# Kernel optimization log

Measured on AMD Instinct MI355X. Metric: run time of the kernel, lower is better.

Reference implementation:

```python
import jax, jax.numpy as jnp
import numpy as np

B, L, D, C, NL = 32, 512, 768, 97, 2  # batch, seq_len, hidden, class_nums, gat_layers


def setup_inputs() -> dict:
    key = jax.random.key(0)
    ks = jax.random.split(key, 16)

    def n(k, shape, scale=0.02):
        return jax.random.normal(k, shape, dtype=jnp.float32) * scale

    return dict(
        x=n(ks[0], (B, L, D), 1.0),                 # encoder output
        pos1=jnp.ones((B, L), jnp.float32),          # entity-1 position mask
        pos2=jnp.ones((B, L), jnp.float32),          # entity-2 position mask
        mask=jnp.ones((B, L), jnp.int32),            # attention mask (1 = keep)
        emb=n(ks[1], (C, D), 1.0),                   # relation label embedding table
        rel_w=n(ks[2], (D, D)), rel_b=jnp.zeros((D,), jnp.float32),
        # per-layer, per-RA (axis1: 0=ra1, 1=ra2) parameters
        qw=n(ks[3], (NL, 2, D, D)), qb=jnp.zeros((NL, 2, D), jnp.float32),
        kw=n(ks[4], (NL, 2, D, D)), kb=jnp.zeros((NL, 2, D), jnp.float32),
        vw=n(ks[5], (NL, 2, D, D)), vb=jnp.zeros((NL, 2, D), jnp.float32),
        sw=n(ks[6], (NL, 2, 2 * D)), sb=jnp.zeros((NL, 2), jnp.float32),   # score: Linear(2d,1)
        gw=n(ks[7], (NL, 2, 2 * D)), gb=jnp.zeros((NL, 2), jnp.float32),   # gate:  Linear(2d,1)
        fc1_w=n(ks[8], (3 * D, D)), fc1_b=jnp.zeros((D,), jnp.float32),
        fc2_w=n(ks[9], (D,)), fc2_b=jnp.zeros((), jnp.float32),
    )


def _relation_attention(p, x, qw, qb, kw, kb, vw, vb, sw, sb, gw, gb, mask):
    # p: (b, c, d) queries; x: (b, l, d) keys/values
    d = p.shape[-1]
    q = jnp.einsum('bcd,de->bce', p, qw) + qb          # (b, c, d)
    k = jnp.einsum('bld,de->ble', x, kw) + kb          # (b, l, d)
    # score = Linear(concat([q_i, k_j])) is separable: q@sw[:d] + k@sw[d:] + sb
    score = (q @ sw[:d])[:, :, None] + (k @ sw[d:])[:, None, :] + sb  # (b, c, l)
    if mask is not None:
        score = jnp.where(mask[:, None, :] == 0, jnp.float32(-1e9), score)
    attn = jax.nn.softmax(score, axis=2)
    v = jnp.einsum('bld,de->ble', x, vw) + vb          # (b, l, d)
    out = jnp.einsum('bcl,bld->bcd', attn, v) + p      # (b, c, d)
    # gate = sigmoid(Linear(concat([out, p]))), also separable
    g = jax.nn.sigmoid(out @ gw[:d] + p @ gw[d:] + gb)[..., None]
    return g * out + (1.0 - g) * p


def reference(x, pos1, pos2, mask, emb, rel_w, rel_b,
              qw, qb, kw, kb, vw, vb, sw, sb, gw, gb,
              fc1_w, fc1_b, fc2_w, fc2_b):
    b, d = x.shape[0], x.shape[-1]
    # p = relation(embedding(arange(C))) broadcast over batch
    p = emb @ rel_w + rel_b                            # (C, d)
    p = jnp.broadcast_to(p[None], (b,) + p.shape)      # (b, C, d)

    for li in range(qw.shape[0]):
        x = _relation_attention(x, p, qw[li, 0], qb[li, 0], kw[li, 0], kb[li, 0],
                                vw[li, 0], vb[li, 0], sw[li, 0], sb[li, 0],
                                gw[li, 0], gb[li, 0], None) + x
        p = _relation_attention(p, x, qw[li, 1], qb[li, 1], kw[li, 1], kb[li, 1],
                                vw[li, 1], vb[li, 1], sw[li, 1], sb[li, 1],
                                gw[li, 1], gb[li, 1], mask) + p

    def pool_avg(pos):
        return jnp.sum(x * pos[:, :, None], axis=1) / jnp.sum(pos, axis=1)[:, None]

    e1 = pool_avg(pos1)                                # (b, d)
    e2 = pool_avg(pos2)                                # (b, d)
    cshape = p.shape                                   # (b, C, d)
    pc = jnp.concatenate([p,
                          jnp.broadcast_to(e1[:, None, :], cshape),
                          jnp.broadcast_to(e2[:, None, :], cshape)], axis=2)  # (b, C, 3d)
    h = jnp.tanh(pc @ fc1_w + fc1_b)                   # (b, C, d)
    logits = jax.nn.sigmoid(h @ fc2_w + fc2_b)         # (b, C)
    pred = jnp.argmax(logits, axis=1)                  # (b,)
    return logits, pred
```

## Files before the change

kernel.cpp:

```cpp
#include <hip/hip_runtime.h>
#include <math.h>

#define NBLK 512
#define NTHR 256
static const int Bb = 32, Ls = 512, Dd = 768, Cc = 97;

struct KArgs {
    const float *x0, *pos1, *pos2;
    const int* mask;
    const float *emb, *rel_w, *rel_b, *kw, *vw, *vb, *sw, *gw, *gb;
    const float *fc1w, *fc1b, *fc2w, *fc2b;
    float* out;
    float *p0b, *pp, *sc, *avx1, *avx2, *av1, *av2, *aw1, *aw2, *S0, *S1, *xp1, *xp2, *geb;
    float *kvecs, *pdots, *g1buf, *xd, *gx1, *gx2, *awb;
    float* zbase;
    int zcount;
};

__device__ __forceinline__ float sigm(float x) { return 1.f / (1.f + expf(-x)); }

__device__ __forceinline__ float wred(float v) {
#pragma unroll
    for (int o = 32; o > 0; o >>= 1) v += __shfl_down(v, o, 64);
    return v;
}

__device__ __forceinline__ float blk_sum4(float v, float* shr) {
    v = wred(v);
    int t = threadIdx.x;
    if ((t & 63) == 0) shr[t >> 6] = v;
    __syncthreads();
    float r = shr[0] + shr[1] + shr[2] + shr[3];
    __syncthreads();
    return r;
}

__device__ void sgemm_dev(const float* __restrict__ A, const float* __restrict__ W,
                          const float* __restrict__ bias, float* __restrict__ C,
                          int M, int N, int K, int KC, int bx, int by, int bz,
                          float* As, float* Ws) {
    int tid = threadIdx.x;
    int tx = tid & 15, ty = tid >> 4;
    int bn = bx * 64, bm = by * 64;
    int kb = bz * KC;
    int arow = tid >> 2, akq = (tid & 3) << 2;
    int wrow = tid >> 4, wcol = (tid & 15) << 2;
    int gar = bm + arow;
    bool aval = gar < M;
    const float* Ap = A + (size_t)gar * K + kb + akq;
    const float* Wp = W + (size_t)(kb + wrow) * N + bn + wcol;
    float acc[4][4] = {{0.f}};
    float4 a4 = make_float4(0.f, 0.f, 0.f, 0.f);
    if (aval) a4 = *(const float4*)Ap;
    float4 w4 = *(const float4*)Wp;
    for (int k0 = 0; k0 < KC; k0 += 16) {
        __syncthreads();
        As[(akq + 0) * 64 + arow] = a4.x; As[(akq + 1) * 64 + arow] = a4.y;
        As[(akq + 2) * 64 + arow] = a4.z; As[(akq + 3) * 64 + arow] = a4.w;
        *(float4*)&Ws[wrow * 64 + wcol] = w4;
        __syncthreads();
        if (k0 + 16 < KC) {
            if (aval) a4 = *(const float4*)(Ap + k0 + 16);
            w4 = *(const float4*)(Wp + (size_t)(k0 + 16) * N);
        }
#pragma unroll
        for (int kk = 0; kk < 16; ++kk) {
            float4 a = *(const float4*)&As[kk * 64 + (ty << 2)];
            float4 b = *(const float4*)&Ws[kk * 64 + (tx << 2)];
            acc[0][0]+=a.x*b.x; acc[0][1]+=a.x*b.y; acc[0][2]+=a.x*b.z; acc[0][3]+=a.x*b.w;
            acc[1][0]+=a.y*b.x; acc[1][1]+=a.y*b.y; acc[1][2]+=a.y*b.z; acc[1][3]+=a.y*b.w;
            acc[2][0]+=a.z*b.x; acc[2][1]+=a.z*b.y; acc[2][2]+=a.z*b.z; acc[2][3]+=a.z*b.w;
            acc[3][0]+=a.w*b.x; acc[3][1]+=a.w*b.y; acc[3][2]+=a.w*b.z; acc[3][3]+=a.w*b.w;
        }
    }
    int gc = bn + (tx << 2);
    float4 bz4 = make_float4(0.f, 0.f, 0.f, 0.f);
    if (bz == 0 && bias) bz4 = *(const float4*)(bias + gc);
#pragma unroll
    for (int i = 0; i < 4; ++i) {
        int gr = bm + (ty << 2) + i;
        if (gr < M) {
            float* cp = C + (size_t)gr * N + gc;
            atomicAdd(cp + 0, acc[i][0] + bz4.x); atomicAdd(cp + 1, acc[i][1] + bz4.y);
            atomicAdd(cp + 2, acc[i][2] + bz4.z); atomicAdd(cp + 3, acc[i][3] + bz4.w);
        }
    }
}

__device__ void attn_gemv(const KArgs& a, int phase, int jlin,
                          float* xs, float* lw, float* shr) {
    int t = threadIdx.x;
    int jt = jlin % 3, b = (jlin / 3) % 32, kseg = jlin / 96;
    float v = -3.0e38f, g1 = 0.f;
    if (t < Cc) {
        if (phase == 0) v = a.pdots[t];
        else {
            g1 = sigm(a.pdots[194 + t] + a.sc[128 + b] + a.gb[1]);
            v = 2.f * a.pdots[97 + t] + g1 * a.sc[160 + b];
        }
    }
    if (phase == 1 && jt == 0 && kseg == 0 && t < Cc) a.g1buf[(size_t)b * Cc + t] = g1;
    float m = v;
#pragma unroll
    for (int o = 32; o > 0; o >>= 1) m = fmaxf(m, __shfl_down(m, o, 64));
    if ((t & 63) == 0) shr[t >> 6] = m;
    __syncthreads();
    m = fmaxf(fmaxf(shr[0], shr[1]), fmaxf(shr[2], shr[3]));
    __syncthreads();
    float e = (t < Cc) ? expf(v - m) : 0.f;
    float s = blk_sum4(e, shr);
    float wc = e / s;
    if (t < Cc) lw[t] = wc;
    float cg1 = blk_sum4(wc * g1, shr);
    float alpha = (phase == 0) ? 1.f : 2.f;
    if (t < 96) {
        int d = kseg * 96 + t;
        const float* pc = a.p0b + d;
        float acc2 = 0.f;
#pragma unroll 4
        for (int c = 0; c < Cc; ++c) acc2 += lw[c] * pc[(size_t)c * Dd];
        float val = alpha * acc2;
        if (phase == 1) val += cg1 * a.av1[(size_t)b * Dd + d];
        xs[t] = val;
    }
    __syncthreads();
    const float* W = a.vw + (size_t)(phase == 0 ? 0 : 2) * Dd * Dd;
    const float* bias = a.vb + (phase == 0 ? 0 : 2) * Dd;
    float* outp = (phase == 0) ? a.avx1 : a.avx2;
    int j = jt * 256 + t;
    float acc = (kseg == 0) ? bias[j] : 0.f;
    const float* wp = W + (size_t)(kseg * 96) * Dd + j;
#pragma unroll 8
    for (int dd = 0; dd < 96; ++dd) acc += xs[dd] * wp[(size_t)dd * Dd];
    atomicAdd(&outp[(size_t)b * Dd + j], acc);
    const float* da[4]; const float* db[4]; int nd; float* dout;
    if (phase == 0) {
        da[0]=a.gw;          db[0]=nullptr;
        da[1]=a.kvecs+Dd;    db[1]=nullptr;
        da[2]=a.gw+3072;     db[2]=a.gw+3840;
        da[3]=a.kvecs+3*Dd;  db[3]=nullptr;
        nd = 4; dout = a.sc;
    } else {
        da[0]=a.gw+3072;     db[0]=nullptr;
        da[1]=a.kvecs+3*Dd;  db[1]=nullptr;
        nd = 2; dout = a.sc + 224;
    }
    for (int vv = 0; vv < nd; ++vv) {
        float wv = da[vv][j] + (db[vv] ? db[vv][j] : 0.f);
        float p = blk_sum4(acc * wv, shr);
        if (t == 0) atomicAdd(&dout[vv * 32 + b], p);
    }
}

__device__ void mm_dev(const KArgs& a, int jlin, const float* S, float gamma,
                       const float* avA, const float* coefA, float multA,
                       const float* avB, const float* coefB, float multB,
                       const float* W, const float* bias, float* outp,
                       int ndots, const float* d0a, const float* d0b,
                       const float* d1a, const float* d2a, const float* d2b,
                       float* dout, float* xs, float* shr) {
    int t = threadIdx.x;
    int jt = jlin % 3, b = (jlin / 3) % 32, kseg = jlin / 96;
    if (t < 96) {
        int d = kseg * 96 + t;
        float v = gamma * S[(size_t)b * Dd + d];
        if (avA) v += multA * coefA[b] * avA[(size_t)b * Dd + d];
        if (avB) v += multB * coefB[b] * avB[(size_t)b * Dd + d];
        xs[t] = v;
    }
    __syncthreads();
    int j = jt * 256 + t;
    float acc = (kseg == 0 && bias) ? bias[j] : 0.f;
    const float* wp = W + (size_t)(kseg * 96) * Dd + j;
#pragma unroll 8
    for (int dd = 0; dd < 96; ++dd) acc += xs[dd] * wp[(size_t)dd * Dd];
    atomicAdd(&outp[(size_t)b * Dd + j], acc);
    if (ndots > 0) {
        float wv = d0a[j] + (d0b ? d0b[j] : 0.f);
        float p = blk_sum4(acc * wv, shr);
        if (t == 0) atomicAdd(&dout[b], p);
    }
    if (ndots > 1) {
        float p = blk_sum4(acc * d1a[j], shr);
        if (t == 0) atomicAdd(&dout[32 + b], p);
    }
    if (ndots > 2) {
        float wv = d2a[j] + (d2b ? d2b[j] : 0.f);
        float p = blk_sum4(acc * wv, shr);
        if (t == 0) atomicAdd(&dout[64 + b], p);
    }
}

__device__ void ge_dev(const KArgs& a, int jlin, float* xs, float* xs2) {
    int t = threadIdx.x;
    int jt = jlin % 3, b = (jlin / 3) % 32, kseg = jlin / 96;
    if (t < 96) {
        int d = kseg * 96 + t;
        float a1 = a.avx1[(size_t)b * Dd + d], a2 = a.avx2[(size_t)b * Dd + d];
        xs[t]  = (4.f * a.xp1[(size_t)b * Dd + d] + 2.f * a.sc[448 + b] * a1 + a.sc[480 + b] * a2) * a.sc[576 + b];
        xs2[t] = (4.f * a.xp2[(size_t)b * Dd + d] + 2.f * a.sc[512 + b] * a1 + a.sc[544 + b] * a2) * a.sc[608 + b];
    }
    __syncthreads();
    int j = jt * 256 + t;
    float a1 = 0.f, a2 = 0.f;
    const float* w1 = a.fc1w + (size_t)(Dd + kseg * 96) * Dd + j;
    const float* w2 = a.fc1w + (size_t)(2 * Dd + kseg * 96) * Dd + j;
#pragma unroll 8
    for (int dd = 0; dd < 96; ++dd) {
        a1 += xs[dd] * w1[(size_t)dd * Dd];
        a2 += xs2[dd] * w2[(size_t)dd * Dd];
    }
    float res = a1 + a2 + (kseg == 0 ? a.fc1b[j] : 0.f);
    atomicAdd(&a.geb[(size_t)b * Dd + j], res);
}

__device__ void aw_dual_dev(const KArgs& a, int jlin, float* xs, float* xs2) {
    int t = threadIdx.x;
    int jt = jlin % 3, b = (jlin / 3) % 32, kseg = jlin / 96;
    if (t < 96) {
        int d = kseg * 96 + t;
        xs[t]  = a.av1[(size_t)b * Dd + d];
        xs2[t] = a.av2[(size_t)b * Dd + d];
    }
    __syncthreads();
    int j = jt * 256 + t;
    float a1 = 0.f, a2 = 0.f;
    const float* wp = a.fc1w + (size_t)(kseg * 96) * Dd + j;
#pragma unroll 8
    for (int dd = 0; dd < 96; ++dd) {
        float w = wp[(size_t)dd * Dd];
        a1 += xs[dd] * w;
        a2 += xs2[dd] * w;
    }
    atomicAdd(&a.aw1[(size_t)b * Dd + j], a1);
    atomicAdd(&a.aw2[(size_t)b * Dd + j], a2);
}

__device__ void softgate_dev(const KArgs& a, int phase, int b, float* shr) {
    int t = threadIdx.x;
    float ks[2], ga[2] = {0.f, 0.f}, gb2[2] = {0.f, 0.f};
#pragma unroll
    for (int i = 0; i < 2; ++i) {
        int l = t + (i << 8);
        size_t r = (size_t)b * Ls + l;
        float4 x = *(const float4*)(a.xd + r * 4);
        if (phase == 0) {
            float g = sigm(x.x + a.sc[b] + a.gb[0]);
            a.gx1[r] = g;
            ga[i] = g;
            ks[i] = 2.f * x.y + g * a.sc[32 + b];
        } else {
            float gp = a.gx1[r];
            float g = sigm(2.f * x.z + gp * a.sc[64 + b] + a.sc[224 + b] + a.gb[2]);
            a.gx2[r] = g;
            ga[i] = gp; gb2[i] = g;
            ks[i] = 4.f * x.w + 2.f * gp * a.sc[96 + b] + g * a.sc[256 + b];
        }
        if (a.mask[r] == 0) ks[i] = -1e9f;
    }
    float mx = fmaxf(ks[0], ks[1]);
#pragma unroll
    for (int o = 32; o > 0; o >>= 1) mx = fmaxf(mx, __shfl_down(mx, o, 64));
    if ((t & 63) == 0) shr[t >> 6] = mx;
    __syncthreads();
    mx = fmaxf(fmaxf(shr[0], shr[1]), fmaxf(shr[2], shr[3]));
    __syncthreads();
    float e0 = expf(ks[0] - mx), e1 = expf(ks[1] - mx);
    float s = blk_sum4(e0 + e1, shr);
    float inv = 1.f / s;
    float w0 = e0 * inv, w1 = e1 * inv;
    a.awb[(size_t)b * Ls + t] = w0;
    a.awb[(size_t)b * Ls + t + 256] = w1;
    float ca = blk_sum4(w0 * ga[0] + w1 * ga[1], shr);
    if (phase == 0) {
        if (t == 0) a.sc[320 + b] = ca;
    } else {
        if (t == 0) a.sc[352 + b] = ca;
        float cb = blk_sum4(w0 * gb2[0] + w1 * gb2[1], shr);
        if (t == 0) a.sc[384 + b] = cb;
        float q1a = a.pos1[(size_t)b * Ls + t], q1b = a.pos1[(size_t)b * Ls + t + 256];
        float q2a = a.pos2[(size_t)b * Ls + t], q2b = a.pos2[(size_t)b * Ls + t + 256];
        float s1 = blk_sum4(q1a + q1b, shr);
        float s2 = blk_sum4(q2a + q2b, shr);
        float c11 = blk_sum4(q1a * ga[0] + q1b * ga[1], shr);
        float c12 = blk_sum4(q1a * gb2[0] + q1b * gb2[1], shr);
        float c21 = blk_sum4(q2a * ga[0] + q2b * ga[1], shr);
        float c22 = blk_sum4(q2a * gb2[0] + q2b * gb2[1], shr);
        if (t == 0) {
            a.sc[448 + b] = c11; a.sc[480 + b] = c12;
            a.sc[512 + b] = c21; a.sc[544 + b] = c22;
            a.sc[576 + b] = 1.f / s1; a.sc[608 + b] = 1.f / s2;
        }
    }
}

__device__ void passX_dev(const KArgs& a, int blk, float* S, bool dopos) {
    int t = threadIdx.x;
    if (t >= 192) return;
    int b = blk >> 4, seg = blk & 15, l0 = seg * 32;
    int d4 = t << 2;
    const float* xb = a.x0 + ((size_t)b * Ls + l0) * Dd + d4;
    const float* wb = a.awb + (size_t)b * Ls + l0;
    float4 as = make_float4(0.f,0.f,0.f,0.f);
    float4 a1 = make_float4(0.f,0.f,0.f,0.f);
    float4 a2 = make_float4(0.f,0.f,0.f,0.f);
    for (int l = 0; l < 32; ++l) {
        float4 xv = *(const float4*)(xb + (size_t)l * Dd);
        float wv = wb[l];
        as.x += wv*xv.x; as.y += wv*xv.y; as.z += wv*xv.z; as.w += wv*xv.w;
        if (dopos) {
            float q1 = a.pos1[(size_t)b * Ls + l0 + l], q2 = a.pos2[(size_t)b * Ls + l0 + l];
            a1.x += q1*xv.x; a1.y += q1*xv.y; a1.z += q1*xv.z; a1.w += q1*xv.w;
            a2.x += q2*xv.x; a2.y += q2*xv.y; a2.z += q2*xv.z; a2.w += q2*xv.w;
        }
    }
    float* ds = S + (size_t)b * Dd + d4;
    atomicAdd(ds+0, as.x); atomicAdd(ds+1, as.y); atomicAdd(ds+2, as.z); atomicAdd(ds+3, as.w);
    if (dopos) {
        float* d1 = a.xp1 + (size_t)b * Dd + d4;
        float* d2 = a.xp2 + (size_t)b * Dd + d4;
        atomicAdd(d1+0, a1.x); atomicAdd(d1+1, a1.y); atomicAdd(d1+2, a1.z); atomicAdd(d1+3, a1.w);
        atomicAdd(d2+0, a2.x); atomicAdd(d2+1, a2.y); atomicAdd(d2+2, a2.z); atomicAdd(d2+3, a2.w);
    }
}

__global__ __launch_bounds__(NTHR) void k_zero_kvec(KArgs a) {
    int blk = blockIdx.x, t = threadIdx.x;
    int wv_ = t >> 6, lane = t & 63;
    for (size_t i = (size_t)blk * NTHR + t; i < (size_t)a.zcount; i += (size_t)NBLK * NTHR)
        a.zbase[i] = 0.f;
    int g = blk * 4 + wv_;
    for (int rep = 0; rep < 2; ++rep) {
        int dot = g + rep * 2048;
        if (dot < 3072) {
            int idx = dot / Dd, d = dot - idx * Dd;
            const float* row = a.kw + ((size_t)idx * Dd + d) * Dd;
            const float* swk = a.sw + (size_t)idx * 2 * Dd + Dd;
            float sA = 0.f;
            for (int j = lane; j < Dd; j += 64) sA += row[j] * swk[j];
            sA = wred(sA);
            if (lane == 0) a.kvecs[dot] = sA;
        }
    }
}

__global__ __launch_bounds__(NTHR) void k_gemm1(KArgs a) {
    __shared__ float As[1024], Ws[1024];
    int blk = blockIdx.x;
    sgemm_dev(a.emb, a.rel_w, a.rel_b, a.p0b, Cc, Dd, Dd, 96,
              blk % 12, (blk / 12) % 2, blk / 24, As, Ws);
}

__global__ __launch_bounds__(NTHR) void k_prep2(KArgs a) {
    __shared__ float As[1024], Ws[1024];
    int blk = blockIdx.x, t = threadIdx.x;
    int wv_ = t >> 6, lane = t & 63;
    if (blk < 96) {
        sgemm_dev(a.p0b, a.fc1w, nullptr, a.pp, Cc, Dd, Dd, 192,
                  blk % 12, (blk / 12) % 2, blk / 24, As, Ws);
    } else if (blk < 128) {
        int g2 = (blk - 96) * 4 + wv_;
        for (int k = 0; k < 4; ++k) {
            int j = g2 + k * 128;
            if (k == 3) { if (g2 >= 4) break; j = 384 + g2; }
            if (j >= 388) continue;
            int vv = j / Cc, r = j - vv * Cc;
            const float* va; const float* vb2 = nullptr;
            if (vv == 0) va = a.kvecs;
            else if (vv == 1) va = a.kvecs + 2 * Dd;
            else if (vv == 2) { va = a.gw + 1536; vb2 = a.gw + 2304; }
            else { va = a.gw + 4608; vb2 = a.gw + 5376; }
            const float* row = a.p0b + (size_t)r * Dd;
            float sA = 0.f;
            for (int jj = lane; jj < Dd; jj += 64)
                sA += row[jj] * (va[jj] + (vb2 ? vb2[jj] : 0.f));
            sA = wred(sA);
            if (lane == 0) a.pdots[j] = sA;
        }
    } else {
        float4 gs0[3], k1r[3], gs2[3], k3r[3];
#pragma unroll
        for (int k = 0; k < 3; ++k) {
            int d = (lane << 2) + k * 256;
            float4 ga = *(const float4*)(a.gw + d);
            float4 gbv = *(const float4*)(a.gw + 768 + d);
            gs0[k] = make_float4(ga.x+gbv.x, ga.y+gbv.y, ga.z+gbv.z, ga.w+gbv.w);
            k1r[k] = *(const float4*)(a.kvecs + 768 + d);
            float4 g2a = *(const float4*)(a.gw + 3072 + d);
            float4 g2b = *(const float4*)(a.gw + 3840 + d);
            gs2[k] = make_float4(g2a.x+g2b.x, g2a.y+g2b.y, g2a.z+g2b.z, g2a.w+g2b.w);
            k3r[k] = *(const float4*)(a.kvecs + 2304 + d);
        }
        int gwv = (blk - 128) * 4 + wv_;
        for (int r = gwv; r < Bb * Ls; r += 1536) {
            const float* xr = a.x0 + (size_t)r * Dd;
            float s0 = 0.f, s1 = 0.f, s2 = 0.f, s3 = 0.f;
#pragma unroll
            for (int k = 0; k < 3; ++k) {
                float4 xv = *(const float4*)(xr + (lane << 2) + k * 256);
                s0 += xv.x*gs0[k].x + xv.y*gs0[k].y + xv.z*gs0[k].z + xv.w*gs0[k].w;
                s1 += xv.x*k1r[k].x + xv.y*k1r[k].y + xv.z*k1r[k].z + xv.w*k1r[k].w;
                s2 += xv.x*gs2[k].x + xv.y*gs2[k].y + xv.z*gs2[k].z + xv.w*gs2[k].w;
                s3 += xv.x*k3r[k].x + xv.y*k3r[k].y + xv.z*k3r[k].z + xv.w*k3r[k].w;
            }
            s0 = wred(s0); s1 = wred(s1); s2 = wred(s2); s3 = wred(s3);
            if (lane == 0) {
                float4 o4 = make_float4(s0, s1, s2, s3);
                *(float4*)(a.xd + (size_t)r * 4) = o4;
            }
        }
    }
}

__global__ __launch_bounds__(NTHR) void k_attn(KArgs a, int phase) {
    __shared__ float xs[96], lw[128], shr[16];
    attn_gemv(a, phase, blockIdx.x, xs, lw, shr);
}

__global__ __launch_bounds__(NTHR) void k_softgate(KArgs a, int phase) {
    __shared__ float shr[16];
    softgate_dev(a, phase, blockIdx.x, shr);
}

__global__ __launch_bounds__(NTHR) void k_passX0(KArgs a) {
    passX_dev(a, blockIdx.x, a.S0, true);
}

__global__ __launch_bounds__(NTHR) void k_mm0(KArgs a) {
    __shared__ float xs[96], shr[16];
    mm_dev(a, blockIdx.x, a.S0, 2.f, a.avx1, a.sc + 320, 1.f, nullptr, nullptr, 0.f,
           a.vw + (size_t)1 * Dd * Dd, a.vb + Dd, a.av1,
           3, a.gw + 1536, nullptr, a.kvecs + 2 * Dd, a.gw + 4608, a.gw + 5376,
           a.sc + 128, xs, shr);
}

__global__ __launch_bounds__(NTHR) void k_passX1ge(KArgs a) {
    __shared__ float xs[96], xs2[96];
    int blk = blockIdx.x;
    if (blk < 512) passX_dev(a, blk, a.S1, false);
    else ge_dev(a, blk - 512, xs, xs2);
}

__global__ __launch_bounds__(NTHR) void k_mm1(KArgs a) {
    __shared__ float xs[96], shr[16];
    mm_dev(a, blockIdx.x, a.S1, 4.f, a.avx1, a.sc + 352, 2.f, a.avx2, a.sc + 384, 1.f,
           a.vw + (size_t)3 * Dd * Dd, a.vb + 3 * Dd, a.av2,
           1, a.gw + 4608, nullptr, nullptr, nullptr, nullptr,
           a.sc + 288, xs, shr);
}

__global__ __launch_bounds__(NTHR) void k_awdual(KArgs a) {
    __shared__ float xs[96], xs2[96];
    aw_dual_dev(a, blockIdx.x, xs, xs2);
}

__global__ __launch_bounds__(NTHR) void k_logits(KArgs a) {
    __shared__ float shr[16];
    int blk = blockIdx.x, t = threadIdx.x;
    for (int r = blk; r < Bb * Cc; r += NBLK) {
        int b = r / Cc, c = r - b * Cc;
        float g1 = a.g1buf[r];
        float g2 = sigm(2.f * a.pdots[291 + c] + g1 * a.sc[192 + b] + a.sc[288 + b] + a.gb[3]);
        float ssum = 0.f;
#pragma unroll
        for (int sseg = 0; sseg < 3; ++sseg) {
            int d = t + sseg * 256;
            float h = tanhf(4.f * a.pp[(size_t)c * Dd + d]
                          + 2.f * g1 * a.aw1[(size_t)b * Dd + d]
                          + g2 * a.aw2[(size_t)b * Dd + d]
                          + a.geb[(size_t)b * Dd + d]);
            ssum += h * a.fc2w[d];
        }
        float tt = blk_sum4(ssum, shr);
        if (t == 0) a.out[r] = sigm(tt + a.fc2b[0]);
    }
}

__global__ void k_argmax(KArgs a) {
    int t = threadIdx.x;
    if (t < Bb) {
        const float* row = a.out + (size_t)t * Cc;
        float best = row[0];
        int bi = 0;
        for (int c = 1; c < Cc; ++c) {
            float v = row[c];
            if (v > best) { best = v; bi = c; }
        }
        a.out[Bb * Cc + t] = (float)bi;
    }
}

extern "C" void kernel_launch(void* const* d_in, const int* in_sizes, int n_in,
                              void* d_out, int out_size, void* d_ws, size_t ws_size,
                              hipStream_t stream) {
    KArgs ka;
    ka.x0    = (const float*)d_in[0];
    ka.pos1  = (const float*)d_in[1];
    ka.pos2  = (const float*)d_in[2];
    ka.mask  = (const int*)d_in[3];
    ka.emb   = (const float*)d_in[4];
    ka.rel_w = (const float*)d_in[5];
    ka.rel_b = (const float*)d_in[6];
    ka.kw    = (const float*)d_in[9];
    ka.vw    = (const float*)d_in[11];
    ka.vb    = (const float*)d_in[12];
    ka.sw    = (const float*)d_in[13];
    ka.gw    = (const float*)d_in[15];
    ka.gb    = (const float*)d_in[16];
    ka.fc1w  = (const float*)d_in[17];
    ka.fc1b  = (const float*)d_in[18];
    ka.fc2w  = (const float*)d_in[19];
    ka.fc2b  = (const float*)d_in[20];
    ka.out   = (float*)d_out;

    float* ws = (float*)d_ws;
    size_t off = 0;
    const size_t PD = (size_t)Cc * Dd;
    const size_t BD = (size_t)Bb * Dd;
    ka.p0b  = ws + off; off += PD;
    ka.pp   = ws + off; off += PD;
    ka.sc   = ws + off; off += 640;
    ka.avx1 = ws + off; off += BD;
    ka.avx2 = ws + off; off += BD;
    ka.av1  = ws + off; off += BD;
    ka.av2  = ws + off; off += BD;
    ka.aw1  = ws + off; off += BD;
    ka.aw2  = ws + off; off += BD;
    ka.S0   = ws + off; off += BD;
    ka.S1   = ws + off; off += BD;
    ka.xp1  = ws + off; off += BD;
    ka.xp2  = ws + off; off += BD;
    ka.geb  = ws + off; off += BD;
    ka.zbase = ws;
    ka.zcount = (int)off;
    ka.kvecs = ws + off; off += (size_t)4 * Dd;
    ka.pdots = ws + off; off += 388;
    ka.g1buf = ws + off; off += (size_t)Bb * Cc;
    ka.xd    = ws + off; off += (size_t)Bb * Ls * 4;
    ka.gx1   = ws + off; off += (size_t)Bb * Ls;
    ka.gx2   = ws + off; off += (size_t)Bb * Ls;
    ka.awb   = ws + off; off += (size_t)Bb * Ls;

    k_zero_kvec<<<NBLK, NTHR, 0, stream>>>(ka);
    k_gemm1<<<192, NTHR, 0, stream>>>(ka);
    k_prep2<<<NBLK, NTHR, 0, stream>>>(ka);
    k_attn<<<768, NTHR, 0, stream>>>(ka, 0);
    k_softgate<<<32, NTHR, 0, stream>>>(ka, 0);
    k_passX0<<<NBLK, NTHR, 0, stream>>>(ka);
    k_mm0<<<768, NTHR, 0, stream>>>(ka);
    k_attn<<<768, NTHR, 0, stream>>>(ka, 1);
    k_softgate<<<32, NTHR, 0, stream>>>(ka, 1);
    k_passX1ge<<<1280, NTHR, 0, stream>>>(ka);
    k_mm1<<<768, NTHR, 0, stream>>>(ka);
    k_awdual<<<768, NTHR, 0, stream>>>(ka);
    k_logits<<<NBLK, NTHR, 0, stream>>>(ka);
    k_argmax<<<1, 64, 0, stream>>>(ka);
}
```

Baseline: 339.1 us.

## Fuse all stages into one cooperative persistent kernel with grid syncs

```diff
diff --git a/kernel.cpp b/kernel.cpp
--- a/kernel.cpp
+++ b/kernel.cpp
@@ -1,6 +1,10 @@
 #include <hip/hip_runtime.h>
+#include <hip/hip_cooperative_groups.h>
 #include <math.h>
 
+namespace cg = cooperative_groups;
+
+#define GRID 512
 #define NBLK 512
 #define NTHR 256
 static const int Bb = 32, Ls = 512, Dd = 768, Cc = 97;
@@ -150,6 +154,7 @@
         float p = blk_sum4(acc * wv, shr);
         if (t == 0) atomicAdd(&dout[vv * 32 + b], p);
     }
+    __syncthreads();
 }
 
 __device__ void mm_dev(const KArgs& a, int jlin, const float* S, float gamma,
@@ -189,11 +194,13 @@
         float p = blk_sum4(acc * wv, shr);
         if (t == 0) atomicAdd(&dout[64 + b], p);
     }
+    __syncthreads();
 }
 
 __device__ void ge_dev(const KArgs& a, int jlin, float* xs, float* xs2) {
     int t = threadIdx.x;
     int jt = jlin % 3, b = (jlin / 3) % 32, kseg = jlin / 96;
+    __syncthreads();
     if (t < 96) {
         int d = kseg * 96 + t;
         float a1 = a.avx1[(size_t)b * Dd + d], a2 = a.avx2[(size_t)b * Dd + d];
@@ -217,6 +224,7 @@
 __device__ void aw_dual_dev(const KArgs& a, int jlin, float* xs, float* xs2) {
     int t = threadIdx.x;
     int jt = jlin % 3, b = (jlin / 3) % 32, kseg = jlin / 96;
+    __syncthreads();
     if (t < 96) {
         int d = kseg * 96 + t;
         xs[t]  = a.av1[(size_t)b * Dd + d];
@@ -324,24 +332,177 @@
     }
 }
 
+__device__ void kvec_dot(const KArgs& a, int dot, int lane) {
+    int idx = dot / Dd, d = dot - idx * Dd;
+    const float* row = a.kw + ((size_t)idx * Dd + d) * Dd;
+    const float* swk = a.sw + (size_t)idx * 2 * Dd + Dd;
+    float sA = 0.f;
+    for (int j = lane; j < Dd; j += 64) sA += row[j] * swk[j];
+    sA = wred(sA);
+    if (lane == 0) a.kvecs[dot] = sA;
+}
+
+__device__ void xdots_dev(const KArgs& a, int r0, int rstep, int lane) {
+    float4 gs0[3], k1r[3], gs2[3], k3r[3];
+#pragma unroll
+    for (int k = 0; k < 3; ++k) {
+        int d = (lane << 2) + k * 256;
+        float4 ga = *(const float4*)(a.gw + d);
+        float4 gbv = *(const float4*)(a.gw + 768 + d);
+        gs0[k] = make_float4(ga.x+gbv.x, ga.y+gbv.y, ga.z+gbv.z, ga.w+gbv.w);
+        k1r[k] = *(const float4*)(a.kvecs + 768 + d);
+        float4 g2a = *(const float4*)(a.gw + 3072 + d);
+        float4 g2b = *(const float4*)(a.gw + 3840 + d);
+        gs2[k] = make_float4(g2a.x+g2b.x, g2a.y+g2b.y, g2a.z+g2b.z, g2a.w+g2b.w);
+        k3r[k] = *(const float4*)(a.kvecs + 2304 + d);
+    }
+    for (int r = r0; r < Bb * Ls; r += rstep) {
+        const float* xr = a.x0 + (size_t)r * Dd;
+        float s0 = 0.f, s1 = 0.f, s2 = 0.f, s3 = 0.f;
+#pragma unroll
+        for (int k = 0; k < 3; ++k) {
+            float4 xv = *(const float4*)(xr + (lane << 2) + k * 256);
+            s0 += xv.x*gs0[k].x + xv.y*gs0[k].y + xv.z*gs0[k].z + xv.w*gs0[k].w;
+            s1 += xv.x*k1r[k].x + xv.y*k1r[k].y + xv.z*k1r[k].z + xv.w*k1r[k].w;
+            s2 += xv.x*gs2[k].x + xv.y*gs2[k].y + xv.z*gs2[k].z + xv.w*gs2[k].w;
+            s3 += xv.x*k3r[k].x + xv.y*k3r[k].y + xv.z*k3r[k].z + xv.w*k3r[k].w;
+        }
+        s0 = wred(s0); s1 = wred(s1); s2 = wred(s2); s3 = wred(s3);
+        if (lane == 0) {
+            float4 o4 = make_float4(s0, s1, s2, s3);
+            *(float4*)(a.xd + (size_t)r * 4) = o4;
+        }
+    }
+}
+
+__device__ void pdots_dev(const KArgs& a, int g2, int lane) {
+    for (int k = 0; k < 4; ++k) {
+        int j = g2 + k * 128;
+        if (k == 3) { if (g2 >= 4) break; j = 384 + g2; }
+        if (j >= 388) continue;
+        int vv = j / Cc, r = j - vv * Cc;
+        const float* va; const float* vb2 = nullptr;
+        if (vv == 0) va = a.kvecs;
+        else if (vv == 1) va = a.kvecs + 2 * Dd;
+        else if (vv == 2) { va = a.gw + 1536; vb2 = a.gw + 2304; }
+        else { va = a.gw + 4608; vb2 = a.gw + 5376; }
+        const float* row = a.p0b + (size_t)r * Dd;
+        float sA = 0.f;
+        for (int jj = lane; jj < Dd; jj += 64)
+            sA += row[jj] * (va[jj] + (vb2 ? vb2[jj] : 0.f));
+        sA = wred(sA);
+        if (lane == 0) a.pdots[j] = sA;
+    }
+}
+
+__device__ void logits_dev(const KArgs& a, int r, float* shr) {
+    int t = threadIdx.x;
+    int b = r / Cc, c = r - b * Cc;
+    float g1 = a.g1buf[r];
+    float g2 = sigm(2.f * a.pdots[291 + c] + g1 * a.sc[192 + b] + a.sc[288 + b] + a.gb[3]);
+    float ssum = 0.f;
+#pragma unroll
+    for (int sseg = 0; sseg < 3; ++sseg) {
+        int d = t + sseg * 256;
+        float h = tanhf(4.f * a.pp[(size_t)c * Dd + d]
+                      + 2.f * g1 * a.aw1[(size_t)b * Dd + d]
+                      + g2 * a.aw2[(size_t)b * Dd + d]
+                      + a.geb[(size_t)b * Dd + d]);
+        ssum += h * a.fc2w[d];
+    }
+    float tt = blk_sum4(ssum, shr);
+    if (t == 0) a.out[r] = sigm(tt + a.fc2b[0]);
+}
+
+__global__ __launch_bounds__(NTHR, 2) void kfused(KArgs a) {
+    __shared__ float As[1024], Ws[1024];
+    __shared__ float xs[96], xs2[96], lw[128], shr[16];
+    cg::grid_group grid = cg::this_grid();
+    const int blk = blockIdx.x, t = threadIdx.x;
+    const int wv_ = t >> 6, lane = t & 63;
+
+    for (size_t i = (size_t)blk * NTHR + t; i < (size_t)a.zcount; i += (size_t)GRID * NTHR)
+        a.zbase[i] = 0.f;
+    for (int dot = blk * 4 + wv_; dot < 3072; dot += GRID * 4)
+        kvec_dot(a, dot, lane);
+    grid.sync();
+
+    if (blk < 192) {
+        sgemm_dev(a.emb, a.rel_w, a.rel_b, a.p0b, Cc, Dd, Dd, 96,
+                  blk % 12, (blk / 12) % 2, blk / 24, As, Ws);
+    } else {
+        xdots_dev(a, (blk - 192) * 4 + wv_, (GRID - 192) * 4, lane);
+    }
+    grid.sync();
+
+    if (blk < 96) {
+        sgemm_dev(a.p0b, a.fc1w, nullptr, a.pp, Cc, Dd, Dd, 192,
+                  blk % 12, (blk / 12) % 2, blk / 24, As, Ws);
+    } else if (blk < 128) {
+        pdots_dev(a, (blk - 96) * 4 + wv_, lane);
+    }
+    grid.sync();
+
+    for (int j = blk; j < 768; j += GRID) attn_gemv(a, 0, j, xs, lw, shr);
+    grid.sync();
+
+    if (blk < 32) softgate_dev(a, 0, blk, shr);
+    grid.sync();
+
+    for (int j = blk; j < 512; j += GRID) passX_dev(a, j, a.S0, true);
+    grid.sync();
+
+    for (int j = blk; j < 768; j += GRID)
+        mm_dev(a, j, a.S0, 2.f, a.avx1, a.sc + 320, 1.f, nullptr, nullptr, 0.f,
+               a.vw + (size_t)1 * Dd * Dd, a.vb + Dd, a.av1,
+               3, a.gw + 1536, nullptr, a.kvecs + 2 * Dd, a.gw + 4608, a.gw + 5376,
+               a.sc + 128, xs, shr);
+    grid.sync();
+
+    for (int j = blk; j < 768; j += GRID) attn_gemv(a, 1, j, xs, lw, shr);
+    grid.sync();
+
+    if (blk < 32) softgate_dev(a, 1, blk, shr);
+    grid.sync();
+
+    for (int w = blk; w < 1280; w += GRID) {
+        if (w < 512) passX_dev(a, w, a.S1, false);
+        else ge_dev(a, w - 512, xs, xs2);
+    }
+    grid.sync();
+
+    for (int j = blk; j < 768; j += GRID)
+        mm_dev(a, j, a.S1, 4.f, a.avx1, a.sc + 352, 2.f, a.avx2, a.sc + 384, 1.f,
+               a.vw + (size_t)3 * Dd * Dd, a.vb + 3 * Dd, a.av2,
+               1, a.gw + 4608, nullptr, nullptr, nullptr, nullptr,
+               a.sc + 288, xs, shr);
+    grid.sync();
+
+    for (int j = blk; j < 768; j += GRID) aw_dual_dev(a, j, xs, xs2);
+    grid.sync();
+
+    for (int r = blk; r < Bb * Cc; r += GRID) logits_dev(a, r, shr);
+    grid.sync();
+
+    if (blk == 0 && t < Bb) {
+        const float* row = a.out + (size_t)t * Cc;
+        float best = row[0];
+        int bi = 0;
+        for (int c = 1; c < Cc; ++c) {
+            float v = row[c];
+            if (v > best) { best = v; bi = c; }
+        }
+        a.out[Bb * Cc + t] = (float)bi;
+    }
+}
+
 __global__ __launch_bounds__(NTHR) void k_zero_kvec(KArgs a) {
     int blk = blockIdx.x, t = threadIdx.x;
     int wv_ = t >> 6, lane = t & 63;
     for (size_t i = (size_t)blk * NTHR + t; i < (size_t)a.zcount; i += (size_t)NBLK * NTHR)
         a.zbase[i] = 0.f;
-    int g = blk * 4 + wv_;
-    for (int rep = 0; rep < 2; ++rep) {
-        int dot = g + rep * 2048;
-        if (dot < 3072) {
-            int idx = dot / Dd, d = dot - idx * Dd;
-            const float* row = a.kw + ((size_t)idx * Dd + d) * Dd;
-            const float* swk = a.sw + (size_t)idx * 2 * Dd + Dd;
-            float sA = 0.f;
-            for (int j = lane; j < Dd; j += 64) sA += row[j] * swk[j];
-            sA = wred(sA);
-            if (lane == 0) a.kvecs[dot] = sA;
-        }
-    }
+    for (int dot = blk * 4 + wv_; dot < 3072; dot += NBLK * 4)
+        kvec_dot(a, dot, lane);
 }
 
 __global__ __launch_bounds__(NTHR) void k_gemm1(KArgs a) {
@@ -359,56 +520,9 @@
         sgemm_dev(a.p0b, a.fc1w, nullptr, a.pp, Cc, Dd, Dd, 192,
                   blk % 12, (blk / 12) % 2, blk / 24, As, Ws);
     } else if (blk < 128) {
-        int g2 = (blk - 96) * 4 + wv_;
-        for (int k = 0; k < 4; ++k) {
-            int j = g2 + k * 128;
-            if (k == 3) { if (g2 >= 4) break; j = 384 + g2; }
-            if (j >= 388) continue;
-            int vv = j / Cc, r = j - vv * Cc;
-            const float* va; const float* vb2 = nullptr;
-            if (vv == 0) va = a.kvecs;
-            else if (vv == 1) va = a.kvecs + 2 * Dd;
-            else if (vv == 2) { va = a.gw + 1536; vb2 = a.gw + 2304; }
-            else { va = a.gw + 4608; vb2 = a.gw + 5376; }
-            const float* row = a.p0b + (size_t)r * Dd;
-            float sA = 0.f;
-            for (int jj = lane; jj < Dd; jj += 64)
-                sA += row[jj] * (va[jj] + (vb2 ? vb2[jj] : 0.f));
-            sA = wred(sA);
-            if (lane == 0) a.pdots[j] = sA;
-        }
+        pdots_dev(a, (blk - 96) * 4 + wv_, lane);
     } else {
-        float4 gs0[3], k1r[3], gs2[3], k3r[3];
-#pragma unroll
-        for (int k = 0; k < 3; ++k) {
-            int d = (lane << 2) + k * 256;
-            float4 ga = *(const float4*)(a.gw + d);
-            float4 gbv = *(const float4*)(a.gw + 768 + d);
-            gs0[k] = make_float4(ga.x+gbv.x, ga.y+gbv.y, ga.z+gbv.z, ga.w+gbv.w);
-            k1r[k] = *(const float4*)(a.kvecs + 768 + d);
-            float4 g2a = *(const float4*)(a.gw + 3072 + d);
-            float4 g2b = *(const float4*)(a.gw + 3840 + d);
-            gs2[k] = make_float4(g2a.x+g2b.x, g2a.y+g2b.y, g2a.z+g2b.z, g2a.w+g2b.w);
-            k3r[k] = *(const float4*)(a.kvecs + 2304 + d);
-        }
-        int gwv = (blk - 128) * 4 + wv_;
-        for (int r = gwv; r < Bb * Ls; r += 1536) {
-            const float* xr = a.x0 + (size_t)r * Dd;
-            float s0 = 0.f, s1 = 0.f, s2 = 0.f, s3 = 0.f;
-#pragma unroll
-            for (int k = 0; k < 3; ++k) {
-                float4 xv = *(const float4*)(xr + (lane << 2) + k * 256);
-                s0 += xv.x*gs0[k].x + xv.y*gs0[k].y + xv.z*gs0[k].z + xv.w*gs0[k].w;
-                s1 += xv.x*k1r[k].x + xv.y*k1r[k].y + xv.z*k1r[k].z + xv.w*k1r[k].w;
-                s2 += xv.x*gs2[k].x + xv.y*gs2[k].y + xv.z*gs2[k].z + xv.w*gs2[k].w;
-                s3 += xv.x*k3r[k].x + xv.y*k3r[k].y + xv.z*k3r[k].z + xv.w*k3r[k].w;
-            }
-            s0 = wred(s0); s1 = wred(s1); s2 = wred(s2); s3 = wred(s3);
-            if (lane == 0) {
-                float4 o4 = make_float4(s0, s1, s2, s3);
-                *(float4*)(a.xd + (size_t)r * 4) = o4;
-            }
-        }
+        xdots_dev(a, (blk - 128) * 4 + wv_, (NBLK - 128) * 4, lane);
     }
 }
 
@@ -456,24 +570,7 @@
 
 __global__ __launch_bounds__(NTHR) void k_logits(KArgs a) {
     __shared__ float shr[16];
-    int blk = blockIdx.x, t = threadIdx.x;
-    for (int r = blk; r < Bb * Cc; r += NBLK) {
-        int b = r / Cc, c = r - b * Cc;
-        float g1 = a.g1buf[r];
-        float g2 = sigm(2.f * a.pdots[291 + c] + g1 * a.sc[192 + b] + a.sc[288 + b] + a.gb[3]);
-        float ssum = 0.f;
-#pragma unroll
-        for (int sseg = 0; sseg < 3; ++sseg) {
-            int d = t + sseg * 256;
-            float h = tanhf(4.f * a.pp[(size_t)c * Dd + d]
-                          + 2.f * g1 * a.aw1[(size_t)b * Dd + d]
-                          + g2 * a.aw2[(size_t)b * Dd + d]
-                          + a.geb[(size_t)b * Dd + d]);
-            ssum += h * a.fc2w[d];
-        }
-        float tt = blk_sum4(ssum, shr);
-        if (t == 0) a.out[r] = sigm(tt + a.fc2b[0]);
-    }
+    for (int r = blockIdx.x; r < Bb * Cc; r += NBLK) logits_dev(a, r, shr);
 }
 
 __global__ void k_argmax(KArgs a) {
@@ -541,18 +638,23 @@
     ka.gx2   = ws + off; off += (size_t)Bb * Ls;
     ka.awb   = ws + off; off += (size_t)Bb * Ls;
 
-    k_zero_kvec<<<NBLK, NTHR, 0, stream>>>(ka);
-    k_gemm1<<<192, NTHR, 0, stream>>>(ka);
-    k_prep2<<<NBLK, NTHR, 0, stream>>>(ka);
-    k_attn<<<768, NTHR, 0, stream>>>(ka, 0);
-    k_softgate<<<32, NTHR, 0, stream>>>(ka, 0);
-    k_passX0<<<NBLK, NTHR, 0, stream>>>(ka);
-    k_mm0<<<768, NTHR, 0, stream>>>(ka);
-    k_attn<<<768, NTHR, 0, stream>>>(ka, 1);
-    k_softgate<<<32, NTHR, 0, stream>>>(ka, 1);
-    k_passX1ge<<<1280, NTHR, 0, stream>>>(ka);
-    k_mm1<<<768, NTHR, 0, stream>>>(ka);
-    k_awdual<<<768, NTHR, 0, stream>>>(ka);
-    k_logits<<<NBLK, NTHR, 0, stream>>>(ka);
-    k_argmax<<<1, 64, 0, stream>>>(ka);
-}
+    void* params[] = { (void*)&ka };
+    hipError_t err = hipLaunchCooperativeKernel((void*)kfused, dim3(GRID), dim3(NTHR),
+                                                params, 0, stream);
+    if (err != hipSuccess) {
+        k_zero_kvec<<<NBLK, NTHR, 0, stream>>>(ka);
+        k_gemm1<<<192, NTHR, 0, stream>>>(ka);
+        k_prep2<<<NBLK, NTHR, 0, stream>>>(ka);
+        k_attn<<<768, NTHR, 0, stream>>>(ka, 0);
+        k_softgate<<<32, NTHR, 0, stream>>>(ka, 0);
+        k_passX0<<<NBLK, NTHR, 0, stream>>>(ka);
+        k_mm0<<<768, NTHR, 0, stream>>>(ka);
+        k_attn<<<768, NTHR, 0, stream>>>(ka, 1);
+        k_softgate<<<32, NTHR, 0, stream>>>(ka, 1);
+        k_passX1ge<<<1280, NTHR, 0, stream>>>(ka);
+        k_mm1<<<768, NTHR, 0, stream>>>(ka);
+        k_awdual<<<768, NTHR, 0, stream>>>(ka);
+        k_logits<<<NBLK, NTHR, 0, stream>>>(ka);
+        k_argmax<<<1, 64, 0, stream>>>(ka);
+    }
+}
```

New measurement: 1.028 ms. 3.03x slower.
